# Performance work log

Hardware: AMD Instinct MI355X
Metric: run time of the kernel (lower is better)

Reference implementation:

```python
import jax, jax.numpy as jnp
import numpy as np

INPUT_CHANNELS = 3

def setup_inputs() -> dict:
    key = jax.random.key(0)
    k1, k2 = jax.random.split(key)
    B, N, C = 16, 4096, 3
    x = jax.random.normal(k1, (B, N, C), dtype=jnp.float32)
    y = jax.random.normal(k2, (B, N, C), dtype=jnp.float32)
    return {"x": x, "y": y}

def reference(x, y):
    # Slice to input_channels (identity here since C == INPUT_CHANNELS)
    x = x[:, :, :INPUT_CHANNELS]
    y = y[:, :, :INPUT_CHANNELS]
    # pdist[b, i, j] = ||x_i||^2 + ||y_j||^2 - 2 x_i . y_j  -> squared euclidean
    x2 = jnp.sum(x * x, axis=-1)  # [B, N]
    y2 = jnp.sum(y * y, axis=-1)  # [B, N]
    zz = jnp.einsum('bic,bjc->bij', x, y)  # [B, N, N]
    pdist = x2[:, :, None] + y2[:, None, :] - 2.0 * zz
    # min over axis 1: nearest x for each y; min over axis 2: nearest y for each x
    loss = jnp.mean(jnp.min(pdist, axis=1)) + jnp.mean(jnp.min(pdist, axis=2))
    return loss
```

## Files before the change

### kernel.cpp

```cpp
#include <hip/hip_runtime.h>
#include <stdint.h>

#define BATCH 16
#define NPTS  4096
#define TOT   (BATCH * NPTS)
#define JSEG  8

typedef float f4 __attribute__((ext_vector_type(4)));
typedef float f32x4 __attribute__((ext_vector_type(4)));
typedef short bh8 __attribute__((ext_vector_type(8)));
typedef uint32_t u32;
typedef unsigned short u16;

__device__ __forceinline__ u16 bfr(float f) {
    union { float f; u32 u; } v; v.f = f;
    u32 r = v.u + 0x7FFF + ((v.u >> 16) & 1);
    return (u16)(r >> 16);
}
__device__ __forceinline__ float bfback(u16 h) {
    union { u32 u; float f; } v; v.u = ((u32)h) << 16; return v.f;
}
#define BF16_ONE ((u16)0x3F80)

#define MIN3r(d, a, b, c) \
    asm("v_min3_f32 %0, %1, %2, %3" : "=v"(d) : "v"(a), "v"(b), "v"(c))


__device__ __forceinline__ void build_arec(float a, float b, float c,
                                           bh8* h0, bh8* h1) {
    float s2 = fmaf(a, a, fmaf(b, b, c * c));
    u16 s2h = bfr(s2);
    u16 s2l = bfr(s2 - bfback(s2h));
    float ax = -2.0f * a, ay = -2.0f * b, az = -2.0f * c;
    u16 ahx = bfr(ax), ahy = bfr(ay), ahz = bfr(az);
    u16 alx = bfr(ax - bfback(ahx));
    u16 aly = bfr(ay - bfback(ahy));
    u16 alz = bfr(az - bfback(ahz));
    union { u16 h[8]; bh8 v; } r0, r1;
    r0.h[0] = ahx; r0.h[1] = ahy; r0.h[2] = ahz;
    r0.h[3] = ahx; r0.h[4] = ahy; r0.h[5] = ahz;
    r0.h[6] = alx; r0.h[7] = aly;
    r1.h[0] = alz; r1.h[1] = s2h; r1.h[2] = s2l;
    r1.h[3] = BF16_ONE; r1.h[4] = BF16_ONE;
    r1.h[5] = 0; r1.h[6] = 0; r1.h[7] = 0;
    *h0 = r0.v; *h1 = r1.v;
}

__device__ __forceinline__ void build_brec(float a, float b, float c,
                                           f4* v0, f4* v1) {
    float s2 = fmaf(a, a, fmaf(b, b, c * c));
    u16 s2h = bfr(s2);
    u16 s2l = bfr(s2 - bfback(s2h));
    u16 yhx = bfr(a), yhy = bfr(b), yhz = bfr(c);
    u16 ylx = bfr(a - bfback(yhx));
    u16 yly = bfr(b - bfback(yhy));
    u16 ylz = bfr(c - bfback(yhz));
    union { u16 h[16]; f4 v[2]; } rec;
    rec.h[0] = yhx;  rec.h[1] = yhy;  rec.h[2] = yhz;
    rec.h[3] = ylx;  rec.h[4] = yly;  rec.h[5] = ylz;
    rec.h[6] = yhx;  rec.h[7] = yhy;
    rec.h[8] = yhz;  rec.h[9] = BF16_ONE; rec.h[10] = BF16_ONE;
    rec.h[11] = s2h; rec.h[12] = s2l;
    rec.h[13] = 0; rec.h[14] = 0; rec.h[15] = 0;
    *v0 = rec.v[0]; *v1 = rec.v[1];
}

#define DSRL(dst, base, imm) \
    asm volatile("ds_read_b128 %0, %1 offset:" imm : "=v"(dst) : "v"(base))

#define WAITL(cnt, slot) do { \
    asm volatile("s_waitcnt lgkmcnt(" cnt ")" : "+v"(slot)); \
    __builtin_amdgcn_sched_barrier(0); \
} while (0)

#define MF8(BB) do { \
    p0 = __builtin_amdgcn_mfma_f32_16x16x32_bf16(af0, BB, zc, 0, 0, 0); \
    p1 = __builtin_amdgcn_mfma_f32_16x16x32_bf16(af1, BB, zc, 0, 0, 0); \
    p2 = __builtin_amdgcn_mfma_f32_16x16x32_bf16(af2, BB, zc, 0, 0, 0); \
    p3 = __builtin_amdgcn_mfma_f32_16x16x32_bf16(af3, BB, zc, 0, 0, 0); \
    p4 = __builtin_amdgcn_mfma_f32_16x16x32_bf16(af4, BB, zc, 0, 0, 0); \
    p5 = __builtin_amdgcn_mfma_f32_16x16x32_bf16(af5, BB, zc, 0, 0, 0); \
    p6 = __builtin_amdgcn_mfma_f32_16x16x32_bf16(af6, BB, zc, 0, 0, 0); \
    p7 = __builtin_amdgcn_mfma_f32_16x16x32_bf16(af7, BB, zc, 0, 0, 0); \
} while (0)

#define EPI1() do { \
    ra0[0]=fminf(ra0[0],p0[0]); ra0[1]=fminf(ra0[1],p0[1]); ra0[2]=fminf(ra0[2],p0[2]); ra0[3]=fminf(ra0[3],p0[3]); \
    ra1[0]=fminf(ra1[0],p1[0]); ra1[1]=fminf(ra1[1],p1[1]); ra1[2]=fminf(ra1[2],p1[2]); ra1[3]=fminf(ra1[3],p1[3]); \
    ra2[0]=fminf(ra2[0],p2[0]); ra2[1]=fminf(ra2[1],p2[1]); ra2[2]=fminf(ra2[2],p2[2]); ra2[3]=fminf(ra2[3],p2[3]); \
    ra3[0]=fminf(ra3[0],p3[0]); ra3[1]=fminf(ra3[1],p3[1]); ra3[2]=fminf(ra3[2],p3[2]); ra3[3]=fminf(ra3[3],p3[3]); \
    ra4[0]=fminf(ra4[0],p4[0]); ra4[1]=fminf(ra4[1],p4[1]); ra4[2]=fminf(ra4[2],p4[2]); ra4[3]=fminf(ra4[3],p4[3]); \
    ra5[0]=fminf(ra5[0],p5[0]); ra5[1]=fminf(ra5[1],p5[1]); ra5[2]=fminf(ra5[2],p5[2]); ra5[3]=fminf(ra5[3],p5[3]); \
    ra6[0]=fminf(ra6[0],p6[0]); ra6[1]=fminf(ra6[1],p6[1]); ra6[2]=fminf(ra6[2],p6[2]); ra6[3]=fminf(ra6[3],p6[3]); \
    ra7[0]=fminf(ra7[0],p7[0]); ra7[1]=fminf(ra7[1],p7[1]); ra7[2]=fminf(ra7[2],p7[2]); ra7[3]=fminf(ra7[3],p7[3]); \
    float t0,t1,t2,t3,t4,t5,t6,t7,t8,t9,t10,u0,u1,u2,u3,cv; \
    MIN3r(t0, p0[0], p0[1], p0[2]); \
    MIN3r(t1, p0[3], p1[0], p1[1]); \
    MIN3r(t2, p1[2], p1[3], p2[0]); \
    MIN3r(t3, p2[1], p2[2], p2[3]); \
    MIN3r(t4, p3[0], p3[1], p3[2]); \
    MIN3r(t5, p3[3], p4[0], p4[1]); \
    MIN3r(t6, p4[2], p4[3], p5[0]); \
    MIN3r(t7, p5[1], p5[2], p5[3]); \
    MIN3r(t8, p6[0], p6[1], p6[2]); \
    MIN3r(t9, p6[3], p7[0], p7[1]); \
    MIN3r(t10, p7[2], p7[3], t0); \
    MIN3r(u0, t1, t2, t3); \
    MIN3r(u1, t4, t5, t6); \
    MIN3r(u2, t7, t8, t9); \
    MIN3r(u3, t10, u0, u1); \
    cv = fminf(u2, u3); \
    asm volatile("ds_min_f32 %0, %1" :: "v"(cma), "v"(cv)); \
    cma += 64; \
} while (0)

__global__ __launch_bounds__(256) void chamfer_mfma(const float* __restrict__ x,
                                                    const float* __restrict__ y,
                                                    float* __restrict__ colpart,
                                                    float* __restrict__ rowpart,
                                                    float* __restrict__ out) {
    constexpr int QLEN = NPTS / JSEG;
    __shared__ u16  Bst[QLEN * 16];
    __shared__ float colmin[QLEN];

    int bid  = blockIdx.x;
    int b    = bid >> 6;
    int ic   = (bid >> 3) & 7;
    int jseg = bid & 7;
    int tid  = threadIdx.x;
    int wv   = tid >> 6, lane = tid & 63;
    int lg   = lane >> 4, lm = lane & 15;

    if (bid == 0 && tid == 0) out[0] = 0.0f;

    int i0 = ic * 512 + wv * 128;
    int j0 = jseg * QLEN;

    {
        const float* ysrc = y + ((size_t)b * NPTS + j0) * 3;
        f4* dst = (f4*)Bst;
        #pragma unroll
        for (int r = 0; r < 2; ++r) {
            int rec = tid * 2 + r;
            float a = ysrc[rec * 3 + 0];
            float bb = ysrc[rec * 3 + 1];
            float c = ysrc[rec * 3 + 2];
            f4 v0, v1;
            build_brec(a, bb, c, &v0, &v1);
            dst[rec * 2 + 0] = v0;
            dst[rec * 2 + 1] = v1;
        }
    }
    for (int i = tid; i < QLEN; i += 256) colmin[i] = 3.4e38f;

    bh8 af0, af1, af2, af3, af4, af5, af6, af7;
    {
        bh8 z8 = {0, 0, 0, 0, 0, 0, 0, 0};
        const float* xsrc = x + ((size_t)b * NPTS + i0 + lm) * 3;
        #define BUILD_AF(af, f) do { \
            float a = xsrc[f * 48 + 0]; \
            float bb = xsrc[f * 48 + 1]; \
            float c = xsrc[f * 48 + 2]; \
            bh8 h0, h1; \
            build_arec(a, bb, c, &h0, &h1); \
            af = (lg == 0) ? h0 : ((lg == 1) ? h1 : z8); \
        } while (0)
        BUILD_AF(af0, 0); BUILD_AF(af1, 1); BUILD_AF(af2, 2); BUILD_AF(af3, 3);
        BUILD_AF(af4, 4); BUILD_AF(af5, 5); BUILD_AF(af6, 6); BUILD_AF(af7, 7);
        #undef BUILD_AF
    }
    __syncthreads();

    u32 lofs = (u32)(uintptr_t)&Bst[0] + ((lg < 2) ? (u32)(lm * 32 + lg * 16) : 0u);
    u32 cma  = (u32)(uintptr_t)&colmin[0] + (u32)lm * 4;

    f32x4 zc = {0.f, 0.f, 0.f, 0.f};
    f32x4 big = {3.4e38f, 3.4e38f, 3.4e38f, 3.4e38f};
    f32x4 ra0 = big, ra1 = big, ra2 = big, ra3 = big;
    f32x4 ra4 = big, ra5 = big, ra6 = big, ra7 = big;
    f32x4 p0, p1, p2, p3, p4, p5, p6, p7;
    bh8 s0, s1, s2, s3;

    DSRL(s0, lofs, "0");    DSRL(s1, lofs, "512");
    DSRL(s2, lofs, "1024"); DSRL(s3, lofs, "1536");

    WAITL("3", s0); MF8(s0); DSRL(s0, lofs, "2048"); EPI1();
    WAITL("4", s1); MF8(s1); DSRL(s1, lofs, "2560"); EPI1();
    WAITL("5", s2); MF8(s2); DSRL(s2, lofs, "3072"); EPI1();
    WAITL("6", s3); MF8(s3); DSRL(s3, lofs, "3584"); EPI1();

    u32 lofs2 = lofs + 4096;
    #pragma unroll 1
    for (int k = 0; k < 6; ++k) {
        WAITL("7", s0); MF8(s0); DSRL(s0, lofs2, "0");    EPI1();
        WAITL("7", s1); MF8(s1); DSRL(s1, lofs2, "512");  EPI1();
        WAITL("7", s2); MF8(s2); DSRL(s2, lofs2, "1024"); EPI1();
        WAITL("7", s3); MF8(s3); DSRL(s3, lofs2, "1536"); EPI1();
        lofs2 += 2048;
    }
    WAITL("7", s0); MF8(s0); EPI1();
    WAITL("6", s1); MF8(s1); EPI1();
    WAITL("5", s2); MF8(s2); EPI1();
    WAITL("4", s3); MF8(s3); EPI1();

    #define RRED(r) { r = fminf(r, __shfl_xor(r, 1)); r = fminf(r, __shfl_xor(r, 2)); \
                      r = fminf(r, __shfl_xor(r, 4)); r = fminf(r, __shfl_xor(r, 8)); }
    float* rp = rowpart + (size_t)jseg * TOT + (size_t)b * NPTS + i0 + lg * 4;
    #define RSTORE(pf, fi) do { \
        float a = pf[0], bq = pf[1], c = pf[2], d = pf[3]; \
        RRED(a) RRED(bq) RRED(c) RRED(d) \
        if (lm == 0) { rp[fi*16 + 0] = a; rp[fi*16 + 1] = bq; \
                       rp[fi*16 + 2] = c; rp[fi*16 + 3] = d; } \
    } while (0)
    RSTORE(ra0, 0); RSTORE(ra1, 1); RSTORE(ra2, 2); RSTORE(ra3, 3);
    RSTORE(ra4, 4); RSTORE(ra5, 5); RSTORE(ra6, 6); RSTORE(ra7, 7);

    __syncthreads();
    for (int j = tid; j < QLEN; j += 256)
        colpart[(size_t)ic * TOT + (size_t)b * NPTS + j0 + j] = colmin[j];
}

__global__ __launch_bounds__(256) void chamfer_pass2(const float* __restrict__ rowpart,
                                                     const float* __restrict__ colpart,
                                                     float* __restrict__ out) {
    int t = blockIdx.x * 256 + threadIdx.x;
    float mr = rowpart[t];
    #pragma unroll
    for (int s = 1; s < JSEG; ++s) mr = fminf(mr, rowpart[(size_t)s * TOT + t]);
    float mc = colpart[t];
    #pragma unroll
    for (int ic = 1; ic < 8; ++ic) mc = fminf(mc, colpart[(size_t)ic * TOT + t]);

    float s = mr + mc;
    #pragma unroll
    for (int off = 32; off; off >>= 1) s += __shfl_down(s, off);
    __shared__ float red[4];
    int lane = threadIdx.x & 63, wid = threadIdx.x >> 6;
    if (lane == 0) red[wid] = s;
    __syncthreads();
    if (threadIdx.x == 0) {
        float tot = (red[0] + red[1]) + (red[2] + red[3]);
        atomicAdd(out, tot * (1.0f / (float)TOT));
    }
}

__global__ __launch_bounds__(256) void chamfer_direct(const float* __restrict__ x,
                                                      const float* __restrict__ y,
                                                      float* __restrict__ out) {
    int blk = blockIdx.x;
    int dir = blk >> 8;
    int t = blk & 255;
    int b = t >> 4;
    int chunk = t & 15;
    const float* __restrict__ P = (dir ? y : x) + (b * NPTS + chunk * 256) * 3;
    const float* __restrict__ Q = (dir ? x : y) + b * NPTS * 3;
    float px = P[threadIdx.x * 3 + 0];
    float py = P[threadIdx.x * 3 + 1];
    float pz = P[threadIdx.x * 3 + 2];
    float b0 = 3.4e38f, b1 = 3.4e38f, b2 = 3.4e38f, b3 = 3.4e38f;
    for (int j = 0; j < NPTS; j += 4) {
        #pragma unroll
        for (int u = 0; u < 4; ++u) {
            float dx = px - Q[(j + u) * 3 + 0];
            float dy = py - Q[(j + u) * 3 + 1];
            float dz = pz - Q[(j + u) * 3 + 2];
            float d = fmaf(dx, dx, fmaf(dy, dy, dz * dz));
            if (u == 0) b0 = fminf(b0, d);
            if (u == 1) b1 = fminf(b1, d);
            if (u == 2) b2 = fminf(b2, d);
            if (u == 3) b3 = fminf(b3, d);
        }
    }
    float best = fminf(fminf(b0, b1), fminf(b2, b3));
    float v = best;
    #pragma unroll
    for (int off = 32; off; off >>= 1) v += __shfl_down(v, off);
    __shared__ float red[4];
    int lane = threadIdx.x & 63, wid = threadIdx.x >> 6;
    if (lane == 0) red[wid] = v;
    __syncthreads();
    if (threadIdx.x == 0) {
        float s = (red[0] + red[1]) + (red[2] + red[3]);
        atomicAdd(out, s * (1.0f / (float)TOT));
    }
}

__global__ void zero_kernel(float* out) { out[0] = 0.0f; }

extern "C" void kernel_launch(void* const* d_in, const int* in_sizes, int n_in,
                              void* d_out, int out_size, void* d_ws, size_t ws_size,
                              hipStream_t stream) {
    const float* x = (const float*)d_in[0];
    const float* y = (const float*)d_in[1];
    float* out = (float*)d_out;

    size_t need = (size_t)4 << 20;
    if (ws_size >= need) {
        float* colpart = (float*)d_ws;
        float* rowpart = (float*)((char*)d_ws + ((size_t)2 << 20));
        hipLaunchKernelGGL(chamfer_mfma, dim3(16 * 8 * JSEG), dim3(256), 0, stream,
                           x, y, colpart, rowpart, out);
        hipLaunchKernelGGL(chamfer_pass2, dim3(TOT / 256), dim3(256), 0, stream,
                           rowpart, colpart, out);
    } else {
        hipLaunchKernelGGL(zero_kernel, dim3(1), dim3(1), 0, stream, out);
        hipLaunchKernelGGL(chamfer_direct, dim3(512), dim3(256), 0, stream, x, y, out);
    }
}
```

Before: 38.95 us.

## Switch to 32x32x16 MFMA tiles and split i-range into 16 chunks

Replaces the eight 16x16x32 bf16 MFMAs per B slice with two 32x32x16 MFMAs. The old form wasted half the K dimension by zeroing two lane groups; the new form uses both 32-lane halves for the K split. The row chunk per block is halved to 256 points, which doubles the grid to 2048 blocks and doubles the column-partial buffers reduced in pass2. The intent is less wasted MFMA work and more parallelism, at the cost of more y staging per block, more partial traffic and a larger workspace requirement.

```diff
diff --git a/kernel.cpp b/kernel.cpp
--- a/kernel.cpp
+++ b/kernel.cpp
@@ -7,7 +7,7 @@
 #define JSEG  8
 
 typedef float f4 __attribute__((ext_vector_type(4)));
-typedef float f32x4 __attribute__((ext_vector_type(4)));
+typedef float f32x16 __attribute__((ext_vector_type(16)));
 typedef short bh8 __attribute__((ext_vector_type(8)));
 typedef uint32_t u32;
 typedef unsigned short u16;
@@ -73,45 +73,52 @@
     __builtin_amdgcn_sched_barrier(0); \
 } while (0)
 
-#define MF8(BB) do { \
-    p0 = __builtin_amdgcn_mfma_f32_16x16x32_bf16(af0, BB, zc, 0, 0, 0); \
-    p1 = __builtin_amdgcn_mfma_f32_16x16x32_bf16(af1, BB, zc, 0, 0, 0); \
-    p2 = __builtin_amdgcn_mfma_f32_16x16x32_bf16(af2, BB, zc, 0, 0, 0); \
-    p3 = __builtin_amdgcn_mfma_f32_16x16x32_bf16(af3, BB, zc, 0, 0, 0); \
-    p4 = __builtin_amdgcn_mfma_f32_16x16x32_bf16(af4, BB, zc, 0, 0, 0); \
-    p5 = __builtin_amdgcn_mfma_f32_16x16x32_bf16(af5, BB, zc, 0, 0, 0); \
-    p6 = __builtin_amdgcn_mfma_f32_16x16x32_bf16(af6, BB, zc, 0, 0, 0); \
-    p7 = __builtin_amdgcn_mfma_f32_16x16x32_bf16(af7, BB, zc, 0, 0, 0); \
-} while (0)
-
-#define EPI1() do { \
-    ra0[0]=fminf(ra0[0],p0[0]); ra0[1]=fminf(ra0[1],p0[1]); ra0[2]=fminf(ra0[2],p0[2]); ra0[3]=fminf(ra0[3],p0[3]); \
-    ra1[0]=fminf(ra1[0],p1[0]); ra1[1]=fminf(ra1[1],p1[1]); ra1[2]=fminf(ra1[2],p1[2]); ra1[3]=fminf(ra1[3],p1[3]); \
-    ra2[0]=fminf(ra2[0],p2[0]); ra2[1]=fminf(ra2[1],p2[1]); ra2[2]=fminf(ra2[2],p2[2]); ra2[3]=fminf(ra2[3],p2[3]); \
-    ra3[0]=fminf(ra3[0],p3[0]); ra3[1]=fminf(ra3[1],p3[1]); ra3[2]=fminf(ra3[2],p3[2]); ra3[3]=fminf(ra3[3],p3[3]); \
-    ra4[0]=fminf(ra4[0],p4[0]); ra4[1]=fminf(ra4[1],p4[1]); ra4[2]=fminf(ra4[2],p4[2]); ra4[3]=fminf(ra4[3],p4[3]); \
-    ra5[0]=fminf(ra5[0],p5[0]); ra5[1]=fminf(ra5[1],p5[1]); ra5[2]=fminf(ra5[2],p5[2]); ra5[3]=fminf(ra5[3],p5[3]); \
-    ra6[0]=fminf(ra6[0],p6[0]); ra6[1]=fminf(ra6[1],p6[1]); ra6[2]=fminf(ra6[2],p6[2]); ra6[3]=fminf(ra6[3],p6[3]); \
-    ra7[0]=fminf(ra7[0],p7[0]); ra7[1]=fminf(ra7[1],p7[1]); ra7[2]=fminf(ra7[2],p7[2]); ra7[3]=fminf(ra7[3],p7[3]); \
-    float t0,t1,t2,t3,t4,t5,t6,t7,t8,t9,t10,u0,u1,u2,u3,cv; \
-    MIN3r(t0, p0[0], p0[1], p0[2]); \
-    MIN3r(t1, p0[3], p1[0], p1[1]); \
-    MIN3r(t2, p1[2], p1[3], p2[0]); \
-    MIN3r(t3, p2[1], p2[2], p2[3]); \
-    MIN3r(t4, p3[0], p3[1], p3[2]); \
-    MIN3r(t5, p3[3], p4[0], p4[1]); \
-    MIN3r(t6, p4[2], p4[3], p5[0]); \
-    MIN3r(t7, p5[1], p5[2], p5[3]); \
-    MIN3r(t8, p6[0], p6[1], p6[2]); \
-    MIN3r(t9, p6[3], p7[0], p7[1]); \
-    MIN3r(t10, p7[2], p7[3], t0); \
-    MIN3r(u0, t1, t2, t3); \
-    MIN3r(u1, t4, t5, t6); \
-    MIN3r(u2, t7, t8, t9); \
-    MIN3r(u3, t10, u0, u1); \
-    cv = fminf(u2, u3); \
+#define FOLD16(ra, p) do { \
+    ra[0]=fminf(ra[0],p[0]);   ra[1]=fminf(ra[1],p[1]); \
+    ra[2]=fminf(ra[2],p[2]);   ra[3]=fminf(ra[3],p[3]); \
+    ra[4]=fminf(ra[4],p[4]);   ra[5]=fminf(ra[5],p[5]); \
+    ra[6]=fminf(ra[6],p[6]);   ra[7]=fminf(ra[7],p[7]); \
+    ra[8]=fminf(ra[8],p[8]);   ra[9]=fminf(ra[9],p[9]); \
+    ra[10]=fminf(ra[10],p[10]); ra[11]=fminf(ra[11],p[11]); \
+    ra[12]=fminf(ra[12],p[12]); ra[13]=fminf(ra[13],p[13]); \
+    ra[14]=fminf(ra[14],p[14]); ra[15]=fminf(ra[15],p[15]); \
+} while (0)
+
+#define TREE16(m, p) do { \
+    float t0,t1,t2,t3,t4,u0,u1; \
+    MIN3r(t0, p[0], p[1], p[2]); \
+    MIN3r(t1, p[3], p[4], p[5]); \
+    MIN3r(t2, p[6], p[7], p[8]); \
+    MIN3r(t3, p[9], p[10], p[11]); \
+    MIN3r(t4, p[12], p[13], p[14]); \
+    MIN3r(u0, t0, t1, t2); \
+    MIN3r(u1, t3, t4, p[15]); \
+    m = fminf(u0, u1); \
+} while (0)
+
+#define TILE(slot, pfbase, pfimm) do { \
+    WAITL_CUR(slot); \
+    p = __builtin_amdgcn_mfma_f32_32x32x16_bf16(af0, slot, zc, 0, 0, 0); \
+    q = __builtin_amdgcn_mfma_f32_32x32x16_bf16(af1, slot, zc, 0, 0, 0); \
+    DSRL(slot, pfbase, pfimm); \
+    float m0, m1, cv; \
+    FOLD16(ra0, p); TREE16(m0, p); \
+    FOLD16(ra1, q); TREE16(m1, q); \
+    cv = fminf(m0, m1); \
     asm volatile("ds_min_f32 %0, %1" :: "v"(cma), "v"(cv)); \
-    cma += 64; \
+    cma += 128; \
+} while (0)
+
+#define TILED(slot) do { \
+    WAITL_CUR(slot); \
+    p = __builtin_amdgcn_mfma_f32_32x32x16_bf16(af0, slot, zc, 0, 0, 0); \
+    q = __builtin_amdgcn_mfma_f32_32x32x16_bf16(af1, slot, zc, 0, 0, 0); \
+    float m0, m1, cv; \
+    FOLD16(ra0, p); TREE16(m0, p); \
+    FOLD16(ra1, q); TREE16(m1, q); \
+    cv = fminf(m0, m1); \
+    asm volatile("ds_min_f32 %0, %1" :: "v"(cma), "v"(cv)); \
+    cma += 128; \
 } while (0)
 
 __global__ __launch_bounds__(256) void chamfer_mfma(const float* __restrict__ x,
@@ -124,16 +131,17 @@
     __shared__ float colmin[QLEN];
 
     int bid  = blockIdx.x;
-    int b    = bid >> 6;
-    int ic   = (bid >> 3) & 7;
+    int b    = bid >> 7;
+    int ic   = (bid >> 3) & 15;
     int jseg = bid & 7;
     int tid  = threadIdx.x;
     int wv   = tid >> 6, lane = tid & 63;
-    int lg   = lane >> 4, lm = lane & 15;
+    int lc   = lane & 31;
+    int hh   = lane >> 5;
 
     if (bid == 0 && tid == 0) out[0] = 0.0f;
 
-    int i0 = ic * 512 + wv * 128;
+    int i0 = ic * 256 + wv * 64;
     int j0 = jseg * QLEN;
 
     {
@@ -153,67 +161,80 @@
     }
     for (int i = tid; i < QLEN; i += 256) colmin[i] = 3.4e38f;
 
-    bh8 af0, af1, af2, af3, af4, af5, af6, af7;
+    bh8 af0, af1;
     {
-        bh8 z8 = {0, 0, 0, 0, 0, 0, 0, 0};
-        const float* xsrc = x + ((size_t)b * NPTS + i0 + lm) * 3;
-        #define BUILD_AF(af, f) do { \
-            float a = xsrc[f * 48 + 0]; \
-            float bb = xsrc[f * 48 + 1]; \
-            float c = xsrc[f * 48 + 2]; \
-            bh8 h0, h1; \
-            build_arec(a, bb, c, &h0, &h1); \
-            af = (lg == 0) ? h0 : ((lg == 1) ? h1 : z8); \
-        } while (0)
-        BUILD_AF(af0, 0); BUILD_AF(af1, 1); BUILD_AF(af2, 2); BUILD_AF(af3, 3);
-        BUILD_AF(af4, 4); BUILD_AF(af5, 5); BUILD_AF(af6, 6); BUILD_AF(af7, 7);
-        #undef BUILD_AF
+        const float* xsrc = x + ((size_t)b * NPTS + i0 + lc) * 3;
+        bh8 h0, h1;
+        build_arec(xsrc[0], xsrc[1], xsrc[2], &h0, &h1);
+        af0 = hh ? h1 : h0;
+        build_arec(xsrc[96], xsrc[97], xsrc[98], &h0, &h1);
+        af1 = hh ? h1 : h0;
     }
     __syncthreads();
 
-    u32 lofs = (u32)(uintptr_t)&Bst[0] + ((lg < 2) ? (u32)(lm * 32 + lg * 16) : 0u);
-    u32 cma  = (u32)(uintptr_t)&colmin[0] + (u32)lm * 4;
-
-    f32x4 zc = {0.f, 0.f, 0.f, 0.f};
-    f32x4 big = {3.4e38f, 3.4e38f, 3.4e38f, 3.4e38f};
-    f32x4 ra0 = big, ra1 = big, ra2 = big, ra3 = big;
-    f32x4 ra4 = big, ra5 = big, ra6 = big, ra7 = big;
-    f32x4 p0, p1, p2, p3, p4, p5, p6, p7;
+    u32 lofs = (u32)(uintptr_t)&Bst[0] + (u32)(lc * 32 + hh * 16);
+    u32 cma  = (u32)(uintptr_t)&colmin[0] + (u32)lc * 4;
+
+    f32x16 zc;
+    #pragma unroll
+    for (int i = 0; i < 16; ++i) zc[i] = 0.0f;
+    f32x16 ra0, ra1;
+    #pragma unroll
+    for (int i = 0; i < 16; ++i) { ra0[i] = 3.4e38f; ra1[i] = 3.4e38f; }
+    f32x16 p, q;
     bh8 s0, s1, s2, s3;
 
-    DSRL(s0, lofs, "0");    DSRL(s1, lofs, "512");
-    DSRL(s2, lofs, "1024"); DSRL(s3, lofs, "1536");
-
-    WAITL("3", s0); MF8(s0); DSRL(s0, lofs, "2048"); EPI1();
-    WAITL("4", s1); MF8(s1); DSRL(s1, lofs, "2560"); EPI1();
-    WAITL("5", s2); MF8(s2); DSRL(s2, lofs, "3072"); EPI1();
-    WAITL("6", s3); MF8(s3); DSRL(s3, lofs, "3584"); EPI1();
-
-    u32 lofs2 = lofs + 4096;
+    DSRL(s0, lofs, "0");    DSRL(s1, lofs, "1024");
+    DSRL(s2, lofs, "2048"); DSRL(s3, lofs, "3072");
+
+    #define WAITL_CUR(sl) WAITL("3", sl)
+    TILE(s0, lofs, "4096");
+    #undef WAITL_CUR
+    #define WAITL_CUR(sl) WAITL("4", sl)
+    TILE(s1, lofs, "5120");
+    #undef WAITL_CUR
+    #define WAITL_CUR(sl) WAITL("5", sl)
+    TILE(s2, lofs, "6144");
+    #undef WAITL_CUR
+    #define WAITL_CUR(sl) WAITL("6", sl)
+    TILE(s3, lofs, "7168");
+    #undef WAITL_CUR
+
+    u32 lofs2 = lofs + 8192;
+    #define WAITL_CUR(sl) WAITL("7", sl)
     #pragma unroll 1
-    for (int k = 0; k < 6; ++k) {
-        WAITL("7", s0); MF8(s0); DSRL(s0, lofs2, "0");    EPI1();
-        WAITL("7", s1); MF8(s1); DSRL(s1, lofs2, "512");  EPI1();
-        WAITL("7", s2); MF8(s2); DSRL(s2, lofs2, "1024"); EPI1();
-        WAITL("7", s3); MF8(s3); DSRL(s3, lofs2, "1536"); EPI1();
-        lofs2 += 2048;
-    }
-    WAITL("7", s0); MF8(s0); EPI1();
-    WAITL("6", s1); MF8(s1); EPI1();
-    WAITL("5", s2); MF8(s2); EPI1();
-    WAITL("4", s3); MF8(s3); EPI1();
-
-    #define RRED(r) { r = fminf(r, __shfl_xor(r, 1)); r = fminf(r, __shfl_xor(r, 2)); \
-                      r = fminf(r, __shfl_xor(r, 4)); r = fminf(r, __shfl_xor(r, 8)); }
-    float* rp = rowpart + (size_t)jseg * TOT + (size_t)b * NPTS + i0 + lg * 4;
-    #define RSTORE(pf, fi) do { \
-        float a = pf[0], bq = pf[1], c = pf[2], d = pf[3]; \
-        RRED(a) RRED(bq) RRED(c) RRED(d) \
-        if (lm == 0) { rp[fi*16 + 0] = a; rp[fi*16 + 1] = bq; \
-                       rp[fi*16 + 2] = c; rp[fi*16 + 3] = d; } \
+    for (int k = 0; k < 2; ++k) {
+        TILE(s0, lofs2, "0");
+        TILE(s1, lofs2, "1024");
+        TILE(s2, lofs2, "2048");
+        TILE(s3, lofs2, "3072");
+        lofs2 += 4096;
+    }
+    TILED(s0);
+    #undef WAITL_CUR
+    #define WAITL_CUR(sl) WAITL("6", sl)
+    TILED(s1);
+    #undef WAITL_CUR
+    #define WAITL_CUR(sl) WAITL("5", sl)
+    TILED(s2);
+    #undef WAITL_CUR
+    #define WAITL_CUR(sl) WAITL("4", sl)
+    TILED(s3);
+    #undef WAITL_CUR
+
+    #define RRED32(v) { v = fminf(v, __shfl_xor(v, 1)); v = fminf(v, __shfl_xor(v, 2)); \
+                        v = fminf(v, __shfl_xor(v, 4)); v = fminf(v, __shfl_xor(v, 8)); \
+                        v = fminf(v, __shfl_xor(v, 16)); }
+    float* rowb = rowpart + (size_t)jseg * TOT + (size_t)b * NPTS + i0 + 4 * hh;
+    #define RFIN(ra, f, r) do { \
+        float v = ra[r]; \
+        RRED32(v) \
+        if (lc == 0) rowb[f * 32 + ((r) >> 2) * 8 + ((r) & 3)] = v; \
     } while (0)
-    RSTORE(ra0, 0); RSTORE(ra1, 1); RSTORE(ra2, 2); RSTORE(ra3, 3);
-    RSTORE(ra4, 4); RSTORE(ra5, 5); RSTORE(ra6, 6); RSTORE(ra7, 7);
+    #pragma unroll
+    for (int r = 0; r < 16; ++r) RFIN(ra0, 0, r);
+    #pragma unroll
+    for (int r = 0; r < 16; ++r) RFIN(ra1, 1, r);
 
     __syncthreads();
     for (int j = tid; j < QLEN; j += 256)
@@ -229,7 +250,7 @@
     for (int s = 1; s < JSEG; ++s) mr = fminf(mr, rowpart[(size_t)s * TOT + t]);
     float mc = colpart[t];
     #pragma unroll
-    for (int ic = 1; ic < 8; ++ic) mc = fminf(mc, colpart[(size_t)ic * TOT + t]);
+    for (int ic = 1; ic < 16; ++ic) mc = fminf(mc, colpart[(size_t)ic * TOT + t]);
 
     float s = mr + mc;
     #pragma unroll
@@ -294,11 +315,11 @@
     const float* y = (const float*)d_in[1];
     float* out = (float*)d_out;
 
-    size_t need = (size_t)4 << 20;
+    size_t need = (size_t)6 << 20;
     if (ws_size >= need) {
         float* colpart = (float*)d_ws;
-        float* rowpart = (float*)((char*)d_ws + ((size_t)2 << 20));
-        hipLaunchKernelGGL(chamfer_mfma, dim3(16 * 8 * JSEG), dim3(256), 0, stream,
+        float* rowpart = (float*)((char*)d_ws + ((size_t)4 << 20));
+        hipLaunchKernelGGL(chamfer_mfma, dim3(16 * 16 * JSEG), dim3(256), 0, stream,
                            x, y, colpart, rowpart, out);
         hipLaunchKernelGGL(chamfer_pass2, dim3(TOT / 256), dim3(256), 0, stream,
                            rowpart, colpart, out);
```

New measurement: 54.99 us. 1.41x slower.
